# Kernel optimization log

Hardware: AMD Instinct MI355X
Metric: run time of the kernel (lower is better)

Reference implementation:

```python
import jax, jax.numpy as jnp
import numpy as np

D_MODEL = 1024
NUM_HEADS = 16
HEAD_DIM = D_MODEL // NUM_HEADS


def setup_inputs() -> dict:
    key = jax.random.key(0)
    ks = jax.random.split(key, 5)
    B, S = 4, 2048
    x = jax.random.normal(ks[0], (B, S, D_MODEL), dtype=jnp.float32)
    scale = 1.0 / np.sqrt(D_MODEL)
    qkv_w = jax.random.normal(ks[1], (3 * D_MODEL, D_MODEL), dtype=jnp.float32) * scale
    qkv_b = jnp.zeros((3 * D_MODEL,), dtype=jnp.float32)
    out_w = jax.random.normal(ks[2], (D_MODEL, D_MODEL), dtype=jnp.float32) * scale
    out_b = jnp.zeros((D_MODEL,), dtype=jnp.float32)
    return {"x": x, "qkv_w": qkv_w, "qkv_b": qkv_b, "out_w": out_w, "out_b": out_b}


def reference(x, qkv_w, qkv_b, out_w, out_b):
    B, S, _ = x.shape
    # qkv projection (torch Linear: x @ W.T + b)
    qkv = x @ qkv_w.T + qkv_b  # [B, S, 3*D]
    q, k, v = jnp.split(qkv, 3, axis=-1)
    # [B, H, S, hd]
    q = q.reshape(B, S, NUM_HEADS, HEAD_DIM).transpose(0, 2, 1, 3)
    k = k.reshape(B, S, NUM_HEADS, HEAD_DIM).transpose(0, 2, 1, 3)
    v = v.reshape(B, S, NUM_HEADS, HEAD_DIM).transpose(0, 2, 1, 3)
    scores = jnp.einsum('bhqd,bhkd->bhqk', q, k) / np.sqrt(HEAD_DIM).astype(np.float32)
    attn = jax.nn.softmax(scores, axis=-1)
    context = jnp.einsum('bhqk,bhkd->bhqd', attn, v)  # [B, H, S, hd]
    context = context.transpose(0, 2, 1, 3).reshape(B, S, D_MODEL)
    return context @ out_w.T + out_b
```

## Files before the change

### kernel.cpp

```cpp
#include <hip/hip_runtime.h>
#include <hip/hip_bf16.h>
#include <math.h>

#define D_MODEL 1024
#define NHEADS  16
#define HDIM    64
#define BATCH   4
#define SLEN    2048
#define MROWS   (BATCH * SLEN)
#define QKV_N   (3 * D_MODEL)

typedef __attribute__((ext_vector_type(8))) short bhalf8;
typedef __attribute__((ext_vector_type(4))) float f32x4;

#if __has_builtin(__builtin_amdgcn_exp2f)
#define EXP2(x) __builtin_amdgcn_exp2f(x)
#else
#define EXP2(x) exp2f(x)
#endif

static __device__ __forceinline__ unsigned short f2bf(float f) {
    unsigned int u = __builtin_bit_cast(unsigned int, f);
    unsigned int r = (u + 0x7FFFu + ((u >> 16) & 1u)) >> 16;
    return (unsigned short)r;
}

static __device__ __forceinline__ unsigned int pack_hi16(float lo, float hi) {
    return __builtin_amdgcn_perm(__builtin_bit_cast(unsigned int, hi),
                                 __builtin_bit_cast(unsigned int, lo),
                                 0x07060302u);
}

static __device__ __forceinline__ void load_lds16(const void* g, void* l) {
    __builtin_amdgcn_global_load_lds(
        (const __attribute__((address_space(1))) void*)g,
        (__attribute__((address_space(3))) void*)l, 16, 0, 0);
}

__global__ __launch_bounds__(256) void cast_f32_bf16(
    const float* __restrict__ in, unsigned short* __restrict__ out, int n)
{
    int i = (blockIdx.x * 256 + threadIdx.x) * 4;
    if (i < n) {
        float4 v = *(const float4*)(in + i);
        ushort4 o;
        o.x = f2bf(v.x); o.y = f2bf(v.y); o.z = f2bf(v.z); o.w = f2bf(v.w);
        *(ushort4*)(out + i) = o;
    }
}

template<bool BF16OUT>
__global__ __launch_bounds__(256) void gemm_mfma_bt(
    const unsigned short* __restrict__ A,
    const unsigned short* __restrict__ W,
    const float* __restrict__ bias,
    void* __restrict__ outv,
    int M, int N, int K, int qcols, float qscale)
{
    __shared__ __align__(16) unsigned short As[128 * 32];
    __shared__ __align__(16) unsigned short Bs[128 * 32];

    const int tid  = threadIdx.x;
    const int bm   = blockIdx.y * 128;
    const int bn   = blockIdx.x * 128;
    const int wave = tid >> 6;
    const int lane = tid & 63;
    const int m16  = lane & 15;
    const int quad = lane >> 4;
    const int wm   = (wave & 1) * 64;
    const int wn   = (wave >> 1) * 64;

    const int r0 = tid >> 2;
    const int s0 = tid & 3;
    const int g0 = (s0 - (r0 >> 1)) & 3;
    const int g1 = (s0 - ((r0 + 64) >> 1)) & 3;

    const size_t arow0 = (size_t)(bm + r0) * K + g0 * 8;
    const size_t arow1 = (size_t)(bm + r0 + 64) * K + g1 * 8;
    const size_t brow0 = (size_t)(bn + r0) * K + g0 * 8;
    const size_t brow1 = (size_t)(bn + r0 + 64) * K + g1 * 8;

    f32x4 acc[4][4];
    f32x4 zero = {0.f, 0.f, 0.f, 0.f};
#pragma unroll
    for (int i = 0; i < 4; ++i)
#pragma unroll
        for (int j = 0; j < 4; ++j) acc[i][j] = zero;

    for (int kt = 0; kt < K; kt += 32) {
        __syncthreads();
        load_lds16(A + arow0 + kt, As + tid * 8);
        load_lds16(A + arow1 + kt, As + 2048 + tid * 8);
        load_lds16(W + brow0 + kt, Bs + tid * 8);
        load_lds16(W + brow1 + kt, Bs + 2048 + tid * 8);
        __asm__ volatile("s_waitcnt vmcnt(0)" ::: "memory");
        __syncthreads();

        bhalf8 af[4], bf[4];
#pragma unroll
        for (int i = 0; i < 4; ++i) {
            int ra = wm + i * 16 + m16;
            int sa = (quad + (ra >> 1)) & 3;
            af[i] = *(const bhalf8*)&As[ra * 32 + sa * 8];
        }
#pragma unroll
        for (int j = 0; j < 4; ++j) {
            int rb = wn + j * 16 + m16;
            int sb = (quad + (rb >> 1)) & 3;
            bf[j] = *(const bhalf8*)&Bs[rb * 32 + sb * 8];
        }
#pragma unroll
        for (int i = 0; i < 4; ++i)
#pragma unroll
            for (int j = 0; j < 4; ++j)
                acc[i][j] = __builtin_amdgcn_mfma_f32_16x16x32_bf16(
                    af[i], bf[j], acc[i][j], 0, 0, 0);
    }

    float bj[4], scj[4];
#pragma unroll
    for (int j = 0; j < 4; ++j) {
        int col = bn + wn + j * 16 + m16;
        bj[j]  = bias[col];
        scj[j] = (col < qcols) ? qscale : 1.0f;
    }

#pragma unroll
    for (int i = 0; i < 4; ++i) {
#pragma unroll
        for (int r = 0; r < 4; ++r) {
            size_t row = (size_t)(bm + wm + i * 16 + quad * 4 + r);
            if (BF16OUT) {
                unsigned short* dst = (unsigned short*)outv + row * N + bn + wn;
#pragma unroll
                for (int j = 0; j < 4; ++j)
                    dst[j * 16 + m16] = f2bf((acc[i][j][r] + bj[j]) * scj[j]);
            } else {
                float* dst = (float*)outv + row * N + bn + wn;
#pragma unroll
                for (int j = 0; j < 4; ++j)
                    dst[j * 16 + m16] = (acc[i][j][r] + bj[j]) * scj[j];
            }
        }
    }
}

__global__ __launch_bounds__(256, 4) void attn_mfma_kernel(
    const unsigned short* __restrict__ qkv, unsigned short* __restrict__ ctx)
{
    const int qt = blockIdx.x;
    const int h  = blockIdx.y;
    const int b  = blockIdx.z;
    const int tid  = threadIdx.x;
    const int wave = tid >> 6;
    const int lane = tid & 63;
    const int m16  = lane & 15;
    const int quad = lane >> 4;

    __shared__ __align__(16) unsigned short K_lds[64 * 64];
    __shared__ __align__(16) unsigned short Vt_lds[64 * 72];
    __shared__ __align__(16) unsigned short QP_lds[4 * 32 * 72];

    const int srow  = tid >> 3;
    const int sslot = tid & 7;

    {
        const unsigned short* qbase =
            qkv + (size_t)(b * SLEN + qt * 128) * QKV_N + h * HDIM;
#pragma unroll
        for (int c = 0; c < 4; ++c) {
            int r = c * 32 + srow;
            int g = (sslot - r) & 7;
            load_lds16(qbase + (size_t)r * QKV_N + g * 8,
                       QP_lds + c * 2048 + tid * 8);
        }
    }
    __asm__ volatile("s_waitcnt vmcnt(0)" ::: "memory");
    __syncthreads();

    bhalf8 qf[2][2];
#pragma unroll
    for (int qi = 0; qi < 2; ++qi) {
        int rq = wave * 32 + qi * 16 + m16;
#pragma unroll
        for (int ks = 0; ks < 2; ++ks) {
            int slot = (ks * 4 + quad + rq) & 7;
            qf[qi][ks] = *(const bhalf8*)&QP_lds[rq * 64 + slot * 8];
        }
    }

    f32x4 zero = {0.f, 0.f, 0.f, 0.f};
    f32x4 oacc[2][4], oacc_l[2];
#pragma unroll
    for (int qi = 0; qi < 2; ++qi) {
        oacc_l[qi] = zero;
#pragma unroll
        for (int dt = 0; dt < 4; ++dt) oacc[qi][dt] = zero;
    }

    bhalf8 ones;
#pragma unroll
    for (int i = 0; i < 8; ++i) ones[i] = (short)0x3F80;

    const int u    = tid & 31;
    const int k0   = (u & 15) | ((u & 16) << 1);
    const int idx0 = (u & 15) * 4 + ((u >> 4) << 1);
    const int vd0  = (tid >> 5) * 8;

    unsigned short* P = &QP_lds[wave * (32 * 72)];

    for (int kt = 0; kt < SLEN / 64; ++kt) {
        __syncthreads();

        {
            const unsigned short* kbase =
                qkv + (size_t)(b * SLEN + kt * 64) * QKV_N + D_MODEL + h * HDIM;
#pragma unroll
            for (int c = 0; c < 2; ++c) {
                int r = c * 32 + srow;
                int g = (sslot - r) & 7;
                load_lds16(kbase + (size_t)r * QKV_N + g * 8,
                           K_lds + c * 2048 + tid * 8);
            }
        }
        {
            const unsigned short* vbase =
                qkv + (size_t)(b * SLEN + kt * 64) * QKV_N + 2 * D_MODEL + h * HDIM;
            uint4 va = *(const uint4*)(vbase + (size_t)k0 * QKV_N + vd0);
            uint4 vb = *(const uint4*)(vbase + (size_t)(k0 + 16) * QKV_N + vd0);
            unsigned int* dst0 = (unsigned int*)&Vt_lds[(vd0 + 0) * 72 + idx0];
            unsigned int* dst1 = (unsigned int*)&Vt_lds[(vd0 + 1) * 72 + idx0];
            dst0[0]            = __builtin_amdgcn_perm(vb.x, va.x, 0x05040100u);
            dst1[0]            = __builtin_amdgcn_perm(vb.x, va.x, 0x07060302u);
            *(unsigned int*)&Vt_lds[(vd0 + 2) * 72 + idx0] = __builtin_amdgcn_perm(vb.y, va.y, 0x05040100u);
            *(unsigned int*)&Vt_lds[(vd0 + 3) * 72 + idx0] = __builtin_amdgcn_perm(vb.y, va.y, 0x07060302u);
            *(unsigned int*)&Vt_lds[(vd0 + 4) * 72 + idx0] = __builtin_amdgcn_perm(vb.z, va.z, 0x05040100u);
            *(unsigned int*)&Vt_lds[(vd0 + 5) * 72 + idx0] = __builtin_amdgcn_perm(vb.z, va.z, 0x07060302u);
            *(unsigned int*)&Vt_lds[(vd0 + 6) * 72 + idx0] = __builtin_amdgcn_perm(vb.w, va.w, 0x05040100u);
            *(unsigned int*)&Vt_lds[(vd0 + 7) * 72 + idx0] = __builtin_amdgcn_perm(vb.w, va.w, 0x07060302u);
        }
        __asm__ volatile("s_waitcnt vmcnt(0)" ::: "memory");
        __syncthreads();

        f32x4 sacc[2][4];
#pragma unroll
        for (int qi = 0; qi < 2; ++qi)
#pragma unroll
            for (int nt = 0; nt < 4; ++nt) sacc[qi][nt] = zero;
#pragma unroll
        for (int ks = 0; ks < 2; ++ks) {
#pragma unroll
            for (int nt = 0; nt < 4; ++nt) {
                int rk = nt * 16 + m16;
                int slot = (ks * 4 + quad + rk) & 7;
                bhalf8 kf = *(const bhalf8*)&K_lds[rk * 64 + slot * 8];
                sacc[0][nt] = __builtin_amdgcn_mfma_f32_16x16x32_bf16(
                    qf[0][ks], kf, sacc[0][nt], 0, 0, 0);
                sacc[1][nt] = __builtin_amdgcn_mfma_f32_16x16x32_bf16(
                    qf[1][ks], kf, sacc[1][nt], 0, 0, 0);
            }
        }

#pragma unroll
        for (int qi = 0; qi < 2; ++qi) {
#pragma unroll
            for (int r = 0; r < 4; ++r) {
                float p0 = EXP2(sacc[qi][0][r]);
                float p1 = EXP2(sacc[qi][1][r]);
                float p2 = EXP2(sacc[qi][2][r]);
                float p3 = EXP2(sacc[qi][3][r]);
                uint2 w;
                w.x = pack_hi16(p0, p1);
                w.y = pack_hi16(p2, p3);
                *(uint2*)&P[(qi * 16 + quad * 4 + r) * 72 + m16 * 4] = w;
            }
        }

        __asm__ volatile("s_waitcnt lgkmcnt(0)" ::: "memory");

#pragma unroll
        for (int ks = 0; ks < 2; ++ks) {
            bhalf8 pf0 = *(const bhalf8*)&P[(m16)      * 72 + ks * 32 + quad * 8];
            bhalf8 pf1 = *(const bhalf8*)&P[(16 + m16) * 72 + ks * 32 + quad * 8];
            oacc_l[0] = __builtin_amdgcn_mfma_f32_16x16x32_bf16(pf0, ones, oacc_l[0], 0, 0, 0);
            oacc_l[1] = __builtin_amdgcn_mfma_f32_16x16x32_bf16(pf1, ones, oacc_l[1], 0, 0, 0);
#pragma unroll
            for (int dt = 0; dt < 4; ++dt) {
                bhalf8 vf = *(const bhalf8*)&Vt_lds[(dt * 16 + m16) * 72 + ks * 32 + quad * 8];
                oacc[0][dt] = __builtin_amdgcn_mfma_f32_16x16x32_bf16(pf0, vf, oacc[0][dt], 0, 0, 0);
                oacc[1][dt] = __builtin_amdgcn_mfma_f32_16x16x32_bf16(pf1, vf, oacc[1][dt], 0, 0, 0);
            }
        }
    }

#pragma unroll
    for (int qi = 0; qi < 2; ++qi) {
#pragma unroll
        for (int r = 0; r < 4; ++r) {
            float inv = 1.0f / oacc_l[qi][r];
            int row = b * SLEN + qt * 128 + wave * 32 + qi * 16 + quad * 4 + r;
            unsigned short* dst = ctx + (size_t)row * D_MODEL + h * HDIM;
#pragma unroll
            for (int dt = 0; dt < 4; ++dt)
                dst[dt * 16 + m16] = f2bf(oacc[qi][dt][r] * inv);
        }
    }
}

extern "C" void kernel_launch(void* const* d_in, const int* in_sizes, int n_in,
                              void* d_out, int out_size, void* d_ws, size_t ws_size,
                              hipStream_t stream)
{
    const float* x     = (const float*)d_in[0];
    const float* qkv_w = (const float*)d_in[1];
    const float* qkv_b = (const float*)d_in[2];
    const float* out_w = (const float*)d_in[3];
    const float* out_b = (const float*)d_in[4];
    float* out = (float*)d_out;

    unsigned short* xbf  = (unsigned short*)d_ws;
    unsigned short* wqkv = xbf  + (size_t)MROWS * D_MODEL;
    unsigned short* wout = wqkv + (size_t)QKV_N * D_MODEL;
    unsigned short* qkv  = wout + (size_t)D_MODEL * D_MODEL;
    unsigned short* ctx  = qkv  + (size_t)MROWS * QKV_N;

    {
        int n;
        n = MROWS * D_MODEL;
        cast_f32_bf16<<<n / 1024, 256, 0, stream>>>(x, xbf, n);
        n = QKV_N * D_MODEL;
        cast_f32_bf16<<<n / 1024, 256, 0, stream>>>(qkv_w, wqkv, n);
        n = D_MODEL * D_MODEL;
        cast_f32_bf16<<<n / 1024, 256, 0, stream>>>(out_w, wout, n);
    }

    const float QSCALE = 0.125f * 1.44269504088896f;

    {
        dim3 grid(QKV_N / 128, MROWS / 128);
        gemm_mfma_bt<true><<<grid, 256, 0, stream>>>(xbf, wqkv, qkv_b, qkv,
                                                     MROWS, QKV_N, D_MODEL,
                                                     D_MODEL, QSCALE);
    }

    {
        dim3 grid(SLEN / 128, NHEADS, BATCH);
        attn_mfma_kernel<<<grid, 256, 0, stream>>>(qkv, ctx);
    }

    {
        dim3 grid(D_MODEL / 128, MROWS / 128);
        gemm_mfma_bt<false><<<grid, 256, 0, stream>>>(ctx, wout, out_b, out,
                                                      MROWS, D_MODEL, D_MODEL,
                                                      0, 1.0f);
    }
}
```

Baseline: 284.2 us.

## Pre-transpose V, double-buffer K/V loads, and enlarge attention query tile

Adds a separate kernel that writes V per head in a transposed, permuted layout so the attention kernel can stream it with async LDS loads instead of doing per-tile register transposes. The attention kernel now double-buffers K and V in LDS, prefetching the next tile while computing the current one, and each block handles 256 queries (64 per wave) so every K/V tile is reused across more queries. The costs are an extra kernel launch with a V round trip through memory, more registers and LDS per block, lower occupancy (launch bounds 2), and half as many attention blocks.

```diff
diff --git a/kernel.cpp b/kernel.cpp
--- a/kernel.cpp
+++ b/kernel.cpp
@@ -145,8 +145,44 @@
     }
 }
 
-__global__ __launch_bounds__(256, 4) void attn_mfma_kernel(
-    const unsigned short* __restrict__ qkv, unsigned short* __restrict__ ctx)
+__global__ __launch_bounds__(256) void transpose_v(
+    const unsigned short* __restrict__ qkv, unsigned short* __restrict__ vT)
+{
+    const int kt = blockIdx.x;
+    const int h  = blockIdx.y;
+    const int b  = blockIdx.z;
+    const int tid = threadIdx.x;
+
+    __shared__ __align__(16) unsigned short Vs[64 * 72];
+
+    {
+        const unsigned short* src = qkv
+            + (size_t)(b * SLEN + kt * 64 + (tid >> 2)) * QKV_N + 2 * D_MODEL + h * HDIM;
+        int c = tid & 3;
+        *(uint4*)&Vs[(tid >> 2) * 72 + c * 8]       = *(const uint4*)(src + c * 8);
+        *(uint4*)&Vs[(tid >> 2) * 72 + (c + 4) * 8] = *(const uint4*)(src + (c + 4) * 8);
+    }
+    __syncthreads();
+
+    const int d = tid >> 2;
+    const int c = tid & 3;
+    unsigned short vals[16];
+#pragma unroll
+    for (int m = 0; m < 16; ++m) {
+        int p = c * 16 + m;
+        int k = ((p & 3) << 4) | (p >> 2);
+        vals[m] = Vs[k * 72 + d];
+    }
+    unsigned short* dst = vT
+        + ((size_t)((b * NHEADS + h) * HDIM + d)) * SLEN + kt * 64 + c * 16;
+    *(uint4*)dst       = *(uint4*)&vals[0];
+    *(uint4*)(dst + 8) = *(uint4*)&vals[8];
+}
+
+__global__ __launch_bounds__(256, 2) void attn_mfma_kernel(
+    const unsigned short* __restrict__ qkv,
+    const unsigned short* __restrict__ vT,
+    unsigned short* __restrict__ ctx)
 {
     const int qt = blockIdx.x;
     const int h  = blockIdx.y;
@@ -157,42 +193,50 @@
     const int m16  = lane & 15;
     const int quad = lane >> 4;
 
-    __shared__ __align__(16) unsigned short K_lds[64 * 64];
-    __shared__ __align__(16) unsigned short Vt_lds[64 * 72];
-    __shared__ __align__(16) unsigned short QP_lds[4 * 32 * 72];
+    __shared__ __align__(16) unsigned short K_lds[2][64 * 64];
+    __shared__ __align__(16) unsigned short V_lds[2][64 * 64];
+    __shared__ __align__(16) unsigned short QP_lds[4 * 64 * 72];
 
     const int srow  = tid >> 3;
     const int sslot = tid & 7;
 
-    {
-        const unsigned short* qbase =
-            qkv + (size_t)(b * SLEN + qt * 128) * QKV_N + h * HDIM;
-#pragma unroll
-        for (int c = 0; c < 4; ++c) {
+    const unsigned short* qbase = qkv + (size_t)(b * SLEN + qt * 256) * QKV_N + h * HDIM;
+    const unsigned short* kbase = qkv + (size_t)(b * SLEN) * QKV_N + D_MODEL + h * HDIM;
+    const unsigned short* vbase = vT + (size_t)((b * NHEADS + h) * HDIM) * SLEN;
+
+#pragma unroll
+    for (int c = 0; c < 8; ++c) {
+        int r = c * 32 + srow;
+        int g = (sslot - r) & 7;
+        load_lds16(qbase + (size_t)r * QKV_N + g * 8, QP_lds + c * 2048 + tid * 8);
+    }
+    {
+#pragma unroll
+        for (int c = 0; c < 2; ++c) {
             int r = c * 32 + srow;
             int g = (sslot - r) & 7;
-            load_lds16(qbase + (size_t)r * QKV_N + g * 8,
-                       QP_lds + c * 2048 + tid * 8);
-        }
-    }
-    __asm__ volatile("s_waitcnt vmcnt(0)" ::: "memory");
+            load_lds16(kbase + (size_t)r * QKV_N + g * 8, &K_lds[0][c * 2048 + tid * 8]);
+            load_lds16(vbase + (size_t)r * SLEN + g * 8,  &V_lds[0][c * 2048 + tid * 8]);
+        }
+    }
     __syncthreads();
 
-    bhalf8 qf[2][2];
-#pragma unroll
-    for (int qi = 0; qi < 2; ++qi) {
-        int rq = wave * 32 + qi * 16 + m16;
+    bhalf8 qf[4][2];
+#pragma unroll
+    for (int qi = 0; qi < 4; ++qi) {
+        int rq = wave * 64 + qi * 16 + m16;
 #pragma unroll
         for (int ks = 0; ks < 2; ++ks) {
             int slot = (ks * 4 + quad + rq) & 7;
             qf[qi][ks] = *(const bhalf8*)&QP_lds[rq * 64 + slot * 8];
         }
     }
+    __syncthreads();
 
     f32x4 zero = {0.f, 0.f, 0.f, 0.f};
-    f32x4 oacc[2][4], oacc_l[2];
-#pragma unroll
-    for (int qi = 0; qi < 2; ++qi) {
+    f32x4 oacc[4][4], oacc_l[4];
+#pragma unroll
+    for (int qi = 0; qi < 4; ++qi) {
         oacc_l[qi] = zero;
 #pragma unroll
         for (int dt = 0; dt < 4; ++dt) oacc[qi][dt] = zero;
@@ -202,73 +246,51 @@
 #pragma unroll
     for (int i = 0; i < 8; ++i) ones[i] = (short)0x3F80;
 
-    const int u    = tid & 31;
-    const int k0   = (u & 15) | ((u & 16) << 1);
-    const int idx0 = (u & 15) * 4 + ((u >> 4) << 1);
-    const int vd0  = (tid >> 5) * 8;
-
-    unsigned short* P = &QP_lds[wave * (32 * 72)];
+    unsigned short* P = &QP_lds[wave * (64 * 72)];
 
     for (int kt = 0; kt < SLEN / 64; ++kt) {
-        __syncthreads();
-
-        {
-            const unsigned short* kbase =
-                qkv + (size_t)(b * SLEN + kt * 64) * QKV_N + D_MODEL + h * HDIM;
+        const int buf = kt & 1;
+
+        if (kt + 1 < SLEN / 64) {
+            const unsigned short* kb = kbase + (size_t)((kt + 1) * 64) * QKV_N;
+            const unsigned short* vb = vbase + (kt + 1) * 64;
 #pragma unroll
             for (int c = 0; c < 2; ++c) {
                 int r = c * 32 + srow;
                 int g = (sslot - r) & 7;
-                load_lds16(kbase + (size_t)r * QKV_N + g * 8,
-                           K_lds + c * 2048 + tid * 8);
-            }
-        }
-        {
-            const unsigned short* vbase =
-                qkv + (size_t)(b * SLEN + kt * 64) * QKV_N + 2 * D_MODEL + h * HDIM;
-            uint4 va = *(const uint4*)(vbase + (size_t)k0 * QKV_N + vd0);
-            uint4 vb = *(const uint4*)(vbase + (size_t)(k0 + 16) * QKV_N + vd0);
-            unsigned int* dst0 = (unsigned int*)&Vt_lds[(vd0 + 0) * 72 + idx0];
-            unsigned int* dst1 = (unsigned int*)&Vt_lds[(vd0 + 1) * 72 + idx0];
-            dst0[0]            = __builtin_amdgcn_perm(vb.x, va.x, 0x05040100u);
-            dst1[0]            = __builtin_amdgcn_perm(vb.x, va.x, 0x07060302u);
-            *(unsigned int*)&Vt_lds[(vd0 + 2) * 72 + idx0] = __builtin_amdgcn_perm(vb.y, va.y, 0x05040100u);
-            *(unsigned int*)&Vt_lds[(vd0 + 3) * 72 + idx0] = __builtin_amdgcn_perm(vb.y, va.y, 0x07060302u);
-            *(unsigned int*)&Vt_lds[(vd0 + 4) * 72 + idx0] = __builtin_amdgcn_perm(vb.z, va.z, 0x05040100u);
-            *(unsigned int*)&Vt_lds[(vd0 + 5) * 72 + idx0] = __builtin_amdgcn_perm(vb.z, va.z, 0x07060302u);
-            *(unsigned int*)&Vt_lds[(vd0 + 6) * 72 + idx0] = __builtin_amdgcn_perm(vb.w, va.w, 0x05040100u);
-            *(unsigned int*)&Vt_lds[(vd0 + 7) * 72 + idx0] = __builtin_amdgcn_perm(vb.w, va.w, 0x07060302u);
-        }
-        __asm__ volatile("s_waitcnt vmcnt(0)" ::: "memory");
-        __syncthreads();
-
-        f32x4 sacc[2][4];
-#pragma unroll
-        for (int qi = 0; qi < 2; ++qi)
-#pragma unroll
-            for (int nt = 0; nt < 4; ++nt) sacc[qi][nt] = zero;
-#pragma unroll
-        for (int ks = 0; ks < 2; ++ks) {
+                load_lds16(kb + (size_t)r * QKV_N + g * 8, &K_lds[buf ^ 1][c * 2048 + tid * 8]);
+                load_lds16(vb + (size_t)r * SLEN + g * 8,  &V_lds[buf ^ 1][c * 2048 + tid * 8]);
+            }
+        }
+
+        bhalf8 kf[2][4];
+#pragma unroll
+        for (int ks = 0; ks < 2; ++ks)
 #pragma unroll
             for (int nt = 0; nt < 4; ++nt) {
                 int rk = nt * 16 + m16;
                 int slot = (ks * 4 + quad + rk) & 7;
-                bhalf8 kf = *(const bhalf8*)&K_lds[rk * 64 + slot * 8];
-                sacc[0][nt] = __builtin_amdgcn_mfma_f32_16x16x32_bf16(
-                    qf[0][ks], kf, sacc[0][nt], 0, 0, 0);
-                sacc[1][nt] = __builtin_amdgcn_mfma_f32_16x16x32_bf16(
-                    qf[1][ks], kf, sacc[1][nt], 0, 0, 0);
-            }
-        }
-
-#pragma unroll
-        for (int qi = 0; qi < 2; ++qi) {
+                kf[ks][nt] = *(const bhalf8*)&K_lds[buf][rk * 64 + slot * 8];
+            }
+
+#pragma unroll
+        for (int qi = 0; qi < 4; ++qi) {
+            f32x4 sacc[4];
+#pragma unroll
+            for (int nt = 0; nt < 4; ++nt) sacc[nt] = zero;
+#pragma unroll
+            for (int ks = 0; ks < 2; ++ks)
+#pragma unroll
+                for (int nt = 0; nt < 4; ++nt)
+                    sacc[nt] = __builtin_amdgcn_mfma_f32_16x16x32_bf16(
+                        qf[qi][ks], kf[ks][nt], sacc[nt], 0, 0, 0);
+
 #pragma unroll
             for (int r = 0; r < 4; ++r) {
-                float p0 = EXP2(sacc[qi][0][r]);
-                float p1 = EXP2(sacc[qi][1][r]);
-                float p2 = EXP2(sacc[qi][2][r]);
-                float p3 = EXP2(sacc[qi][3][r]);
+                float p0 = EXP2(sacc[0][r]);
+                float p1 = EXP2(sacc[1][r]);
+                float p2 = EXP2(sacc[2][r]);
+                float p3 = EXP2(sacc[3][r]);
                 uint2 w;
                 w.x = pack_hi16(p0, p1);
                 w.y = pack_hi16(p2, p3);
@@ -278,27 +300,38 @@
 
         __asm__ volatile("s_waitcnt lgkmcnt(0)" ::: "memory");
 
-#pragma unroll
-        for (int ks = 0; ks < 2; ++ks) {
-            bhalf8 pf0 = *(const bhalf8*)&P[(m16)      * 72 + ks * 32 + quad * 8];
-            bhalf8 pf1 = *(const bhalf8*)&P[(16 + m16) * 72 + ks * 32 + quad * 8];
-            oacc_l[0] = __builtin_amdgcn_mfma_f32_16x16x32_bf16(pf0, ones, oacc_l[0], 0, 0, 0);
-            oacc_l[1] = __builtin_amdgcn_mfma_f32_16x16x32_bf16(pf1, ones, oacc_l[1], 0, 0, 0);
+        bhalf8 vf[2][4];
+#pragma unroll
+        for (int ks = 0; ks < 2; ++ks)
 #pragma unroll
             for (int dt = 0; dt < 4; ++dt) {
-                bhalf8 vf = *(const bhalf8*)&Vt_lds[(dt * 16 + m16) * 72 + ks * 32 + quad * 8];
-                oacc[0][dt] = __builtin_amdgcn_mfma_f32_16x16x32_bf16(pf0, vf, oacc[0][dt], 0, 0, 0);
-                oacc[1][dt] = __builtin_amdgcn_mfma_f32_16x16x32_bf16(pf1, vf, oacc[1][dt], 0, 0, 0);
-            }
-        }
-    }
-
-#pragma unroll
-    for (int qi = 0; qi < 2; ++qi) {
+                int rv = dt * 16 + m16;
+                int slot = (ks * 4 + quad + rv) & 7;
+                vf[ks][dt] = *(const bhalf8*)&V_lds[buf][rv * 64 + slot * 8];
+            }
+
+#pragma unroll
+        for (int ks = 0; ks < 2; ++ks)
+#pragma unroll
+            for (int qi = 0; qi < 4; ++qi) {
+                bhalf8 pf = *(const bhalf8*)&P[(qi * 16 + m16) * 72 + ks * 32 + quad * 8];
+                oacc_l[qi] = __builtin_amdgcn_mfma_f32_16x16x32_bf16(
+                    pf, ones, oacc_l[qi], 0, 0, 0);
+#pragma unroll
+                for (int dt = 0; dt < 4; ++dt)
+                    oacc[qi][dt] = __builtin_amdgcn_mfma_f32_16x16x32_bf16(
+                        pf, vf[ks][dt], oacc[qi][dt], 0, 0, 0);
+            }
+
+        __syncthreads();
+    }
+
+#pragma unroll
+    for (int qi = 0; qi < 4; ++qi) {
 #pragma unroll
         for (int r = 0; r < 4; ++r) {
             float inv = 1.0f / oacc_l[qi][r];
-            int row = b * SLEN + qt * 128 + wave * 32 + qi * 16 + quad * 4 + r;
+            int row = b * SLEN + qt * 256 + wave * 64 + qi * 16 + quad * 4 + r;
             unsigned short* dst = ctx + (size_t)row * D_MODEL + h * HDIM;
 #pragma unroll
             for (int dt = 0; dt < 4; ++dt)
@@ -323,6 +356,7 @@
     unsigned short* wout = wqkv + (size_t)QKV_N * D_MODEL;
     unsigned short* qkv  = wout + (size_t)D_MODEL * D_MODEL;
     unsigned short* ctx  = qkv  + (size_t)MROWS * QKV_N;
+    unsigned short* vTb  = ctx  + (size_t)MROWS * D_MODEL;
 
     {
         int n;
@@ -344,8 +378,13 @@
     }
 
     {
-        dim3 grid(SLEN / 128, NHEADS, BATCH);
-        attn_mfma_kernel<<<grid, 256, 0, stream>>>(qkv, ctx);
+        dim3 grid(SLEN / 64, NHEADS, BATCH);
+        transpose_v<<<grid, 256, 0, stream>>>(qkv, vTb);
+    }
+
+    {
+        dim3 grid(SLEN / 256, NHEADS, BATCH);
+        attn_mfma_kernel<<<grid, 256, 0, stream>>>(qkv, vTb, ctx);
     }
 
     {
```

After: 284.7 us. No clear change (+0.2%).
